# Kernel tuning notes

Measured on AMD Instinct MI355X. Metric: run time of the kernel, lower is better.

The kernel has to match this reference:

```python
import jax, jax.numpy as jnp
import numpy as np

N_NODES = 50000
N_EDGES = 600000
D = 128


def setup_inputs() -> dict:
    key = jax.random.key(0)
    ks = jax.random.split(key, 8)
    x = jax.random.normal(ks[0], (N_NODES, D), dtype=jnp.float32)
    edge_index = jax.random.randint(ks[1], (2, N_EDGES), 0, N_NODES, dtype=jnp.int64)
    s = 1.0 / np.sqrt(D)
    W_l1 = jax.random.uniform(ks[2], (D, D), jnp.float32, -s, s)
    W_r1 = jax.random.uniform(ks[3], (D, D), jnp.float32, -s, s)
    b1 = jnp.zeros((D,), jnp.float32)
    W_l2 = jax.random.uniform(ks[4], (D, D), jnp.float32, -s, s)
    W_r2 = jax.random.uniform(ks[5], (D, D), jnp.float32, -s, s)
    b2 = jnp.zeros((D,), jnp.float32)
    return {"x": x, "edge_index": edge_index, "W_l1": W_l1, "W_r1": W_r1,
            "b1": b1, "W_l2": W_l2, "W_r2": W_r2, "b2": b2}


def _sage_conv(x, src, dst, W_l, W_r, b):
    # mean aggregation over incoming edges (src -> dst), PyG SAGEConv semantics
    n = x.shape[0]
    msg = x[src]                                               # [E, D] gather
    agg = jax.ops.segment_sum(msg, dst, num_segments=n)        # [N, D] scatter-add
    cnt = jax.ops.segment_sum(jnp.ones((src.shape[0],), x.dtype), dst, num_segments=n)
    mean = agg / jnp.maximum(cnt, 1.0)[:, None]
    return mean @ W_l + x @ W_r + b


def reference(x, edge_index, W_l1, W_r1, b1, W_l2, W_r2, b2):
    src, dst = edge_index[0], edge_index[1]
    h = jax.nn.relu(_sage_conv(x, src, dst, W_l1, W_r1, b1))
    out = _sage_conv(h, src, dst, W_l2, W_r2, b2)
    return out
```

## Files before the change

### kernel.cpp

```cpp
#include <hip/hip_runtime.h>
#include <hip/hip_bf16.h>

#define N_NODES 50000
#define N_EDGES 600000
#define D 128
#define K2 256
#define MAXDEG 64

#define CVT_BLOCKS   (N_NODES * 16 / 256)
#define BUILD_BLOCKS ((N_EDGES + 255) / 256)
#define PREPW_BLOCKS (2 * D * K2 / 256)
#define PREP_GRID (CVT_BLOCKS + BUILD_BLOCKS + PREPW_BLOCKS)

typedef __bf16 bf16x8 __attribute__((ext_vector_type(8)));
typedef float  f32x16 __attribute__((ext_vector_type(16)));

__device__ __forceinline__ unsigned short f32_to_bf16_rne(float f) {
    unsigned int u = __builtin_bit_cast(unsigned int, f);
    unsigned int r = (u + 0x7fffu + ((u >> 16) & 1u)) >> 16;
    return (unsigned short)r;
}
__device__ __forceinline__ unsigned pk2(float lo, float hi) {
    return (unsigned)f32_to_bf16_rne(lo) | ((unsigned)f32_to_bf16_rne(hi) << 16);
}
__device__ __forceinline__ float bfl(unsigned int u) { return __builtin_bit_cast(float, u << 16); }
__device__ __forceinline__ float bfh(unsigned int u) { return __builtin_bit_cast(float, u & 0xffff0000u); }

__global__ __launch_bounds__(256) void prep_kernel(
    const float* __restrict__ x, const int* __restrict__ ei,
    const float* __restrict__ Wl1, const float* __restrict__ Wr1,
    const float* __restrict__ Wl2, const float* __restrict__ Wr2,
    unsigned short* __restrict__ A0, unsigned short* __restrict__ WT,
    int* __restrict__ counts, int* __restrict__ slots)
{
    const int b = blockIdx.x;
    if (b < CVT_BLOCKS) {
        int idx = b * 256 + threadIdx.x;
        int node = idx >> 4, g = idx & 15;
        const float4* xp = (const float4*)(x + (size_t)node * D + g * 8);
        float4 v0 = xp[0], v1 = xp[1];
        uint4 o;
        o.x = pk2(v0.x, v0.y); o.y = pk2(v0.z, v0.w);
        o.z = pk2(v1.x, v1.y); o.w = pk2(v1.z, v1.w);
        ((uint4*)A0)[(size_t)node * 16 + g] = o;
    } else if (b < CVT_BLOCKS + BUILD_BLOCKS) {
        int e = (b - CVT_BLOCKS) * 256 + threadIdx.x;
        if (e < N_EDGES) {
            int src = ei[e];
            int dst = ei[N_EDGES + e];
            int pos = atomicAdd(&counts[dst], 1);
            if (pos < MAXDEG) slots[(size_t)dst * MAXDEG + pos] = src;
        }
    } else {
        int idx = (b - CVT_BLOCKS - BUILD_BLOCKS) * 256 + threadIdx.x;
        int layer = idx >> 15, rem = idx & 32767;
        int n = rem >> 8, k = rem & 255;
        const float* Wl = layer ? Wl2 : Wl1;
        const float* Wr = layer ? Wr2 : Wr1;
        float v = (k < D) ? Wl[k * D + n] : Wr[(k - D) * D + n];
        WT[((size_t)layer << 15) + n * K2 + k] = f32_to_bf16_rne(v);
    }
}

template <bool RELU, bool OUT_BF16>
__global__ __launch_bounds__(256) void layer_kernel(
    const unsigned short* __restrict__ Xin,
    const int* __restrict__ counts, const int* __restrict__ slots,
    const unsigned short* __restrict__ WT,
    const float* __restrict__ bias,
    unsigned short* __restrict__ Hout,
    float* __restrict__ outf)
{
    __shared__ uint4 As4[32 * 33];
    const int tid = threadIdx.x;
    const int lane = tid & 63;
    const int wv = tid >> 6;
    const int base = blockIdx.x * 32;
    const unsigned* Xu = (const unsigned*)Xin;
    unsigned* As_u = (unsigned*)As4;

    const int f  = lane >> 2;
    const int jd = lane & 3;

    for (int i = 0; i < 8; ++i) {
        const int m = wv * 8 + i;
        const int node = base + m;
        int cnt = 0;
        int sreg = 0;
        if (node < N_NODES) {
            cnt = counts[node];
            sreg = slots[(size_t)node * MAXDEG + lane];
        }
        cnt = __builtin_amdgcn_readfirstlane(min(cnt, MAXDEG));

        float a0 = 0.0f, a1 = 0.0f;
        int e = 0;
        for (; e + 4 <= cnt; e += 4) {
            int s0 = __builtin_amdgcn_readlane(sreg, e);
            int s1 = __builtin_amdgcn_readlane(sreg, e + 1);
            int s2 = __builtin_amdgcn_readlane(sreg, e + 2);
            int s3 = __builtin_amdgcn_readlane(sreg, e + 3);
            unsigned v0 = Xu[(size_t)s0 * 64 + lane];
            unsigned v1 = Xu[(size_t)s1 * 64 + lane];
            unsigned v2 = Xu[(size_t)s2 * 64 + lane];
            unsigned v3 = Xu[(size_t)s3 * 64 + lane];
            a0 += bfl(v0); a1 += bfh(v0);
            a0 += bfl(v1); a1 += bfh(v1);
            a0 += bfl(v2); a1 += bfh(v2);
            a0 += bfl(v3); a1 += bfh(v3);
        }
        for (; e < cnt; ++e) {
            int s0 = __builtin_amdgcn_readlane(sreg, e);
            unsigned v0 = Xu[(size_t)s0 * 64 + lane];
            a0 += bfl(v0); a1 += bfh(v0);
        }
        float inv = 1.0f / fmaxf((float)cnt, 1.0f);
        As_u[(f * 33 + m) * 4 + jd] = pk2(a0 * inv, a1 * inv);
        unsigned xv = 0;
        if (node < N_NODES) xv = Xu[(size_t)node * 64 + lane];
        As_u[((16 + f) * 33 + m) * 4 + jd] = xv;
    }
    __syncthreads();

    const int m = lane & 31;
    const int kg = lane >> 5;
    const int col = wv * 32 + m;
    const uint4* bp = (const uint4*)(WT + (size_t)col * K2 + kg * 8);
    const bf16x8* afrag = (const bf16x8*)As4;

    f32x16 acc = {};
    #pragma unroll
    for (int s = 0; s < 16; ++s) {
        bf16x8 a = afrag[(s * 2 + kg) * 33 + m];
        bf16x8 b = __builtin_bit_cast(bf16x8, bp[s * 2]);
        acc = __builtin_amdgcn_mfma_f32_32x32x16_bf16(a, b, acc, 0, 0, 0);
    }

    const float bc = bias[col];
    const int halfadd = kg * 4;
    #pragma unroll
    for (int r = 0; r < 16; ++r) {
        int rw = base + (r & 3) + 8 * (r >> 2) + halfadd;
        if (rw < N_NODES) {
            float v = acc[r] + bc;
            if (RELU) v = fmaxf(v, 0.0f);
            if (OUT_BF16) Hout[(size_t)rw * D + col] = f32_to_bf16_rne(v);
            else outf[(size_t)rw * D + col] = v;
        }
    }
}

extern "C" void kernel_launch(void* const* d_in, const int* in_sizes, int n_in,
                              void* d_out, int out_size, void* d_ws, size_t ws_size,
                              hipStream_t stream) {
    const float* x   = (const float*)d_in[0];
    const int*   ei  = (const int*)d_in[1];
    const float* Wl1 = (const float*)d_in[2];
    const float* Wr1 = (const float*)d_in[3];
    const float* b1  = (const float*)d_in[4];
    const float* Wl2 = (const float*)d_in[5];
    const float* Wr2 = (const float*)d_in[6];
    const float* b2  = (const float*)d_in[7];
    float* out = (float*)d_out;

    unsigned short* A0 = (unsigned short*)d_ws;
    unsigned short* A1 = A0 + (size_t)N_NODES * D;
    unsigned short* WT = A1 + (size_t)N_NODES * D;
    int* counts = (int*)(WT + 2 * D * K2);
    int* slots  = counts + N_NODES;

    const int layerBlocks = (N_NODES + 31) / 32;

    hipMemsetAsync(counts, 0, N_NODES * sizeof(int), stream);
    prep_kernel<<<PREP_GRID, 256, 0, stream>>>(x, ei, Wl1, Wr1, Wl2, Wr2, A0, WT, counts, slots);

    layer_kernel<true, true><<<layerBlocks, 256, 0, stream>>>(
        A0, counts, slots, WT, b1, A1, nullptr);
    layer_kernel<false, false><<<layerBlocks, 256, 0, stream>>>(
        A1, counts, slots, WT + (size_t)D * K2, b2, nullptr, out);
}
```

Before: 204.4 us.

## Gather neighbor rows with 16-byte loads across four edges per wavefront

The aggregation loop now has each wavefront split into four 16-lane groups. Each lane loads a uint4 (8 bf16) from a different neighbor row, so four edges are gathered per load instruction, then the partial sums are reduced with xor shuffles. Slot and count loads for all eight nodes are hoisted ahead of the loop to expose more memory-level parallelism. The CSR build also processes four edges per thread using int4 loads. The cost is more registers and shuffle work, plus wasted lanes when degrees are not multiples of 16.

```diff
diff --git a/kernel.cpp b/kernel.cpp
--- a/kernel.cpp
+++ b/kernel.cpp
@@ -8,7 +8,7 @@
 #define MAXDEG 64
 
 #define CVT_BLOCKS   (N_NODES * 16 / 256)
-#define BUILD_BLOCKS ((N_EDGES + 255) / 256)
+#define BUILD_BLOCKS ((N_EDGES / 4 + 255) / 256)
 #define PREPW_BLOCKS (2 * D * K2 / 256)
 #define PREP_GRID (CVT_BLOCKS + BUILD_BLOCKS + PREPW_BLOCKS)
 
@@ -44,12 +44,18 @@
         o.z = pk2(v1.x, v1.y); o.w = pk2(v1.z, v1.w);
         ((uint4*)A0)[(size_t)node * 16 + g] = o;
     } else if (b < CVT_BLOCKS + BUILD_BLOCKS) {
-        int e = (b - CVT_BLOCKS) * 256 + threadIdx.x;
-        if (e < N_EDGES) {
-            int src = ei[e];
-            int dst = ei[N_EDGES + e];
-            int pos = atomicAdd(&counts[dst], 1);
-            if (pos < MAXDEG) slots[(size_t)dst * MAXDEG + pos] = src;
+        int e4 = ((b - CVT_BLOCKS) * 256 + threadIdx.x) * 4;
+        if (e4 < N_EDGES) {
+            int4 s4 = *(const int4*)(ei + e4);
+            int4 d4 = *(const int4*)(ei + N_EDGES + e4);
+            int p0 = atomicAdd(&counts[d4.x], 1);
+            int p1 = atomicAdd(&counts[d4.y], 1);
+            int p2 = atomicAdd(&counts[d4.z], 1);
+            int p3 = atomicAdd(&counts[d4.w], 1);
+            if (p0 < MAXDEG) slots[(size_t)d4.x * MAXDEG + p0] = s4.x;
+            if (p1 < MAXDEG) slots[(size_t)d4.y * MAXDEG + p1] = s4.y;
+            if (p2 < MAXDEG) slots[(size_t)d4.z * MAXDEG + p2] = s4.z;
+            if (p3 < MAXDEG) slots[(size_t)d4.w * MAXDEG + p3] = s4.w;
         }
     } else {
         int idx = (b - CVT_BLOCKS - BUILD_BLOCKS) * 256 + threadIdx.x;
@@ -76,49 +82,68 @@
     const int lane = tid & 63;
     const int wv = tid >> 6;
     const int base = blockIdx.x * 32;
-    const unsigned* Xu = (const unsigned*)Xin;
-    unsigned* As_u = (unsigned*)As4;
-
-    const int f  = lane >> 2;
-    const int jd = lane & 3;
-
+    const int g = lane >> 4;
+    const int u = lane & 15;
+    const uint4* X4 = (const uint4*)Xin;
+
+    const int nodeb = base + wv * 8;
+
+    int cntv = 0;
+    {
+        int nn = nodeb + (lane & 7);
+        if (nn < N_NODES) cntv = counts[nn];
+    }
+    int sreg[8];
+    #pragma unroll
+    for (int i = 0; i < 8; ++i) {
+        int node = nodeb + i;
+        sreg[i] = (node < N_NODES) ? slots[(size_t)node * MAXDEG + lane] : 0;
+    }
+
+    #pragma unroll
     for (int i = 0; i < 8; ++i) {
         const int m = wv * 8 + i;
-        const int node = base + m;
-        int cnt = 0;
-        int sreg = 0;
-        if (node < N_NODES) {
-            cnt = counts[node];
-            sreg = slots[(size_t)node * MAXDEG + lane];
-        }
-        cnt = __builtin_amdgcn_readfirstlane(min(cnt, MAXDEG));
-
-        float a0 = 0.0f, a1 = 0.0f;
-        int e = 0;
-        for (; e + 4 <= cnt; e += 4) {
-            int s0 = __builtin_amdgcn_readlane(sreg, e);
-            int s1 = __builtin_amdgcn_readlane(sreg, e + 1);
-            int s2 = __builtin_amdgcn_readlane(sreg, e + 2);
-            int s3 = __builtin_amdgcn_readlane(sreg, e + 3);
-            unsigned v0 = Xu[(size_t)s0 * 64 + lane];
-            unsigned v1 = Xu[(size_t)s1 * 64 + lane];
-            unsigned v2 = Xu[(size_t)s2 * 64 + lane];
-            unsigned v3 = Xu[(size_t)s3 * 64 + lane];
-            a0 += bfl(v0); a1 += bfh(v0);
-            a0 += bfl(v1); a1 += bfh(v1);
-            a0 += bfl(v2); a1 += bfh(v2);
-            a0 += bfl(v3); a1 += bfh(v3);
-        }
-        for (; e < cnt; ++e) {
-            int s0 = __builtin_amdgcn_readlane(sreg, e);
-            unsigned v0 = Xu[(size_t)s0 * 64 + lane];
-            a0 += bfl(v0); a1 += bfh(v0);
-        }
-        float inv = 1.0f / fmaxf((float)cnt, 1.0f);
-        As_u[(f * 33 + m) * 4 + jd] = pk2(a0 * inv, a1 * inv);
-        unsigned xv = 0;
-        if (node < N_NODES) xv = Xu[(size_t)node * 64 + lane];
-        As_u[((16 + f) * 33 + m) * 4 + jd] = xv;
+        const int node = nodeb + i;
+        int cnt = __builtin_amdgcn_readlane(cntv, i);
+        cnt = cnt > MAXDEG ? MAXDEG : cnt;
+
+        float a0 = 0.f, a1 = 0.f, a2 = 0.f, a3 = 0.f;
+        float a4 = 0.f, a5 = 0.f, a6 = 0.f, a7 = 0.f;
+
+        for (int e0 = 0; e0 < cnt; e0 += 16) {
+            #pragma unroll
+            for (int j = 0; j < 4; ++j) {
+                int eidx = e0 + j * 4 + g;
+                int s = __shfl(sreg[i], eidx, 64);
+                uint4 v = {0u, 0u, 0u, 0u};
+                if (eidx < cnt) v = X4[(size_t)s * 16 + u];
+                a0 += bfl(v.x); a1 += bfh(v.x);
+                a2 += bfl(v.y); a3 += bfh(v.y);
+                a4 += bfl(v.z); a5 += bfh(v.z);
+                a6 += bfl(v.w); a7 += bfh(v.w);
+            }
+        }
+
+        a0 += __shfl_xor(a0, 16, 64); a1 += __shfl_xor(a1, 16, 64);
+        a2 += __shfl_xor(a2, 16, 64); a3 += __shfl_xor(a3, 16, 64);
+        a4 += __shfl_xor(a4, 16, 64); a5 += __shfl_xor(a5, 16, 64);
+        a6 += __shfl_xor(a6, 16, 64); a7 += __shfl_xor(a7, 16, 64);
+        a0 += __shfl_xor(a0, 32, 64); a1 += __shfl_xor(a1, 32, 64);
+        a2 += __shfl_xor(a2, 32, 64); a3 += __shfl_xor(a3, 32, 64);
+        a4 += __shfl_xor(a4, 32, 64); a5 += __shfl_xor(a5, 32, 64);
+        a6 += __shfl_xor(a6, 32, 64); a7 += __shfl_xor(a7, 32, 64);
+
+        const float inv = 1.0f / fmaxf((float)cnt, 1.0f);
+        if (g == 0) {
+            uint4 o;
+            o.x = pk2(a0 * inv, a1 * inv); o.y = pk2(a2 * inv, a3 * inv);
+            o.z = pk2(a4 * inv, a5 * inv); o.w = pk2(a6 * inv, a7 * inv);
+            As4[u * 33 + m] = o;
+        } else if (g == 1) {
+            uint4 xv = {0u, 0u, 0u, 0u};
+            if (node < N_NODES) xv = X4[(size_t)node * 16 + u];
+            As4[(16 + u) * 33 + m] = xv;
+        }
     }
     __syncthreads();
 
```

Result: faster. 194.9 us (-4.6%).
